# Performance work log

Hardware: AMD Instinct MI355X
Metric: run time of the kernel (lower is better)

## Reference

```python
import jax, jax.numpy as jnp
import numpy as np

N_NODES = 100000
N_EDGES = 600000
NUM_RELS = 6
NUM_BASES = 6
DIMS = [26, 64, 128, 32]  # in_features -> hidden[0] -> hidden[1] -> X_dim


def _layer(h, etypes, src, dst, V, C, S, b):
    """One basis-decomposed RGCN layer (DGL RelGraphConv semantics).
    h: [N, in]; V: [num_bases, in, out]; C: [num_rels, num_bases];
    S: self-loop weight [in, out]; b: bias [out].
    """
    # compose relation weights from bases: [num_rels, in, out]
    W = jnp.einsum('rb,bio->rio', C, V)
    # transform every node by every relation (cheaper than per-edge [E,in,out])
    h_rel = jnp.einsum('ni,rio->rno', h, W)          # [num_rels, N, out]
    msg = h_rel[etypes, src]                          # [E, out] gather
    agg = jax.ops.segment_sum(msg, dst, num_segments=h.shape[0])  # scatter-add
    return jax.nn.relu(agg + h @ S + b)


def setup_inputs() -> dict:
    key = jax.random.key(0)
    ks = jax.random.split(key, 16)
    inp = {
        'node_feats': jax.random.normal(ks[0], (N_NODES, DIMS[0]), dtype=jnp.float32),
        'src': jax.random.randint(ks[1], (N_EDGES,), 0, N_NODES, dtype=jnp.int32),
        'dst': jax.random.randint(ks[2], (N_EDGES,), 0, N_NODES, dtype=jnp.int32),
        'etypes': jax.random.randint(ks[3], (N_EDGES,), 0, NUM_RELS, dtype=jnp.int32),
    }
    ki = 4
    for l in range(3):
        din, dout = DIMS[l], DIMS[l + 1]
        sc = 1.0 / np.sqrt(din)
        inp[f'V{l+1}'] = jax.random.normal(ks[ki], (NUM_BASES, din, dout), dtype=jnp.float32) * sc
        inp[f'C{l+1}'] = jax.random.normal(ks[ki+1], (NUM_RELS, NUM_BASES), dtype=jnp.float32) * (1.0 / np.sqrt(NUM_BASES))
        inp[f'S{l+1}'] = jax.random.normal(ks[ki+2], (din, dout), dtype=jnp.float32) * sc
        inp[f'b{l+1}'] = jnp.zeros((dout,), dtype=jnp.float32)
        ki += 3
    return inp


def reference(node_feats, src, dst, etypes,
              V1, C1, S1, b1, V2, C2, S2, b2, V3, C3, S3, b3):
    h = _layer(node_feats, etypes, src, dst, V1, C1, S1, b1)
    h = _layer(h, etypes, src, dst, V2, C2, S2, b2)
    h = _layer(h, etypes, src, dst, V3, C3, S3, b3)
    return h
```

## Files before the change

### kernel.cpp

```cpp
#include <hip/hip_runtime.h>

#define NN 100000
#define NE 600000
#define NR 6
#define NB 6
#define NKEY (NN * NR)
#define NCHUNK ((NKEY + 1023) / 1024)

typedef __attribute__((ext_vector_type(8))) short bfrag;
typedef __attribute__((ext_vector_type(8))) unsigned short uvec8;
typedef __attribute__((ext_vector_type(8))) unsigned char ucvec8;
typedef __attribute__((ext_vector_type(4))) float accvec;

__device__ __forceinline__ float bf2f(unsigned short u) {
  union { unsigned int i; float f; } v;
  v.i = ((unsigned int)u) << 16;
  return v.f;
}
__device__ __forceinline__ unsigned short f2bf(float f) {
  union { float f; unsigned int i; } v;
  v.f = f;
  return (unsigned short)((v.i + 0x7FFFu + ((v.i >> 16) & 1u)) >> 16);
}
__device__ __forceinline__ float fp82f(unsigned char u) {
  return __builtin_amdgcn_cvt_f32_fp8((unsigned int)u, 0);
}
__device__ __forceinline__ unsigned char f2fp8(float f) {
  return (unsigned char)(__builtin_amdgcn_cvt_pk_fp8_f32(f, 0.f, 0, false) & 0xff);
}

template <int IN, int OUT, int KS, int NT>
__device__ __forceinline__ void compose_body(int idx, const float* __restrict__ V,
                                             const float* __restrict__ C,
                                             const float* __restrict__ S,
                                             unsigned short* __restrict__ Wf) {
  int lane = idx & 63;
  int t = idx >> 6;
  int nt = t % NT; t /= NT;
  int ks = t % KS; int rel = t / KS;
  int n = nt * 16 + (lane & 15);
  int g = lane >> 4;
  uvec8 o;
#pragma unroll
  for (int i = 0; i < 8; ++i) {
    int k = ks * 32 + g * 8 + i;
    float s = 0.f;
    if (k < IN) {
      if (rel < NR) {
#pragma unroll
        for (int b = 0; b < NB; ++b) s += C[rel * NB + b] * V[((size_t)b * IN + k) * OUT + n];
      } else {
        s = S[(size_t)k * OUT + n];
      }
    }
    o[i] = f2bf(s);
  }
  *(uvec8*)&Wf[(size_t)idx * 8] = o;
}

#define PB_PAD 1563
#define PB_HIST 2344
__global__ __launch_bounds__(256) void prep_kernel(
    const float* __restrict__ nf, unsigned short* __restrict__ hp,
    const int* __restrict__ dst, const int* __restrict__ et, int* __restrict__ cnt,
    const float* V1, const float* C1, const float* S1, unsigned short* W1,
    const float* V2, const float* C2, const float* S2, unsigned short* W2,
    const float* V3, const float* C3, const float* S3, unsigned short* W3) {
  int b = blockIdx.x, tid = threadIdx.x;
  if (b < PB_PAD) {
    int idx = b * 256 + tid;
    if (idx < NN * 4) {
      int n = idx >> 2, c = idx & 3;
      uvec8 o;
#pragma unroll
      for (int i = 0; i < 8; ++i) {
        int k = c * 8 + i;
        o[i] = (k < 26) ? f2bf(nf[n * 26 + k]) : (unsigned short)0;
      }
      *(uvec8*)&hp[(size_t)n * 32 + c * 8] = o;
    }
  } else if (b < PB_PAD + PB_HIST) {
    int e = (b - PB_PAD) * 256 + tid;
    if (e < NE) atomicAdd(&cnt[dst[e] * NR + et[e]], 1);
  } else if (b < PB_PAD + PB_HIST + 7) {
    int idx = (b - PB_PAD - PB_HIST) * 256 + tid;
    compose_body<26, 64, 1, 4>(idx, V1, C1, S1, W1);
  } else if (b < PB_PAD + PB_HIST + 7 + 28) {
    int idx = (b - PB_PAD - PB_HIST - 7) * 256 + tid;
    compose_body<64, 128, 2, 8>(idx, V2, C2, S2, W2);
  } else {
    int idx = (b - PB_PAD - PB_HIST - 35) * 256 + tid;
    compose_body<128, 32, 4, 2>(idx, V3, C3, S3, W3);
  }
}

__global__ void scanA(const int* __restrict__ cnt, int* __restrict__ partial) {
  __shared__ int ts[256];
  int t = threadIdx.x;
  int base = blockIdx.x * 1024 + t * 4;
  int s = 0;
#pragma unroll
  for (int i = 0; i < 4; ++i)
    if (base + i < NKEY) s += cnt[base + i];
  ts[t] = s;
  __syncthreads();
  for (int off = 128; off; off >>= 1) {
    if (t < off) ts[t] += ts[t + off];
    __syncthreads();
  }
  if (t == 0) partial[blockIdx.x] = ts[0];
}

__global__ void scanC2(int* __restrict__ cnt, const int* __restrict__ partial,
                       int* __restrict__ indptr) {
  __shared__ int ts[256];
  int t = threadIdx.x;
  int bid = blockIdx.x;
  int ps = 0;
  for (int i = t; i < bid; i += 256) ps += partial[i];
  ts[t] = ps;
  __syncthreads();
  for (int off = 128; off; off >>= 1) {
    if (t < off) ts[t] += ts[t + off];
    __syncthreads();
  }
  int base = ts[0];
  __syncthreads();

  int bbase = bid * 1024 + t * 4;
  int v[4], s = 0;
#pragma unroll
  for (int i = 0; i < 4; ++i) {
    v[i] = (bbase + i < NKEY) ? cnt[bbase + i] : 0;
    s += v[i];
  }
  ts[t] = s;
  __syncthreads();
  for (int off = 1; off < 256; off <<= 1) {
    int x = (t >= off) ? ts[t - off] : 0;
    __syncthreads();
    ts[t] += x;
    __syncthreads();
  }
  int run = base + ts[t] - s;
#pragma unroll
  for (int i = 0; i < 4; ++i) {
    if (bbase + i < NKEY) {
      indptr[bbase + i] = run;
      cnt[bbase + i] = run;
      run += v[i];
    }
  }
  if (bid == 0 && t == 0) indptr[NKEY] = NE;
}

__global__ void scatter2(const int* __restrict__ et, const int* __restrict__ src,
                         const int* __restrict__ dst, int* __restrict__ cur,
                         int* __restrict__ sidx, int* __restrict__ gidx) {
  int e = blockIdx.x * 256 + threadIdx.x;
  if (e < NE) {
    int r = et[e];
    int s = src[e];
    int key = dst[e] * NR + r;
    int pos = atomicAdd(&cur[key], 1);
    sidx[pos] = s;
    gidx[pos] = r * NN + s;
  }
}

template <int K, int OUT, int MAXE, bool IN_FP8, bool OUT_FP8>
__global__ __launch_bounds__(256, 8) void rgcn_layer_v6(
    const void* __restrict__ hv,
    const unsigned short* __restrict__ Wf,
    const float* __restrict__ bias,
    const int* __restrict__ indptr,
    const int* __restrict__ sidx,
    void* __restrict__ Gout) {
  constexpr int ROWS = 16;
  constexpr int KS = K / 32;
  constexpr int KT = 7 * KS;
  constexpr int NT = OUT / 16;
  constexpr int NTW = NT / 4;
  constexpr int KC = K / 8;
  constexpr int CT = 7 * KC;
  constexpr int ITEMS = (ROWS * CT + 255) / 256;
  constexpr int KP = 7 * K + 8;
  constexpr int MSB = IN_FP8 ? (K + 8) : (2 * K + 16);
  constexpr int ATB = ROWS * KP * 2;
  constexpr int MGB = MAXE * MSB;
  constexpr int LDSB = ATB > MGB ? ATB : MGB;
  constexpr int SITER = MAXE * KC / 256;

  __shared__ __align__(16) char buf[LDSB];
  __shared__ int seg[ROWS * NR + 1];
  unsigned short* A = (unsigned short*)buf;

  const int tid = threadIdx.x;
  const int row0 = blockIdx.x * ROWS;

  if (tid < ROWS * NR + 1) seg[tid] = indptr[row0 * NR + tid];
  __syncthreads();

  const int E0 = seg[0];
  const int E1 = seg[ROWS * NR];

  float sum[ITEMS][8];
#pragma unroll
  for (int i = 0; i < ITEMS; ++i)
#pragma unroll
    for (int q = 0; q < 8; ++q) sum[i][q] = 0.f;

  for (int b0 = E0; b0 < E1; b0 += MAXE) {
    const int bcount = min(MAXE, E1 - b0);
    __syncthreads();

#pragma unroll
    for (int i = 0; i < SITER; ++i) {
      int idx = tid + i * 256;
      int e = idx / KC;
      int c = idx & (KC - 1);
      int ec = min(e, bcount - 1);
      int s = sidx[b0 + ec];
      if constexpr (IN_FP8) {
        *(ucvec8*)&buf[e * MSB + c * 8] =
            *(const ucvec8*)((const unsigned char*)hv + (size_t)s * K + c * 8);
      } else {
        *(uvec8*)&buf[e * MSB + c * 16] =
            *(const uvec8*)((const unsigned short*)hv + (size_t)s * K + c * 8);
      }
    }
    __syncthreads();

#pragma unroll
    for (int i = 0; i < ITEMS; ++i) {
      int idx = tid + i * 256;
      if (idx < ROWS * CT) {
        int row = idx / CT, chunk = idx % CT;
        if (chunk < 6 * KC) {
          int rel = chunk / KC, c = chunk & (KC - 1);
          int beg = seg[row * NR + rel], end = seg[row * NR + rel + 1];
          int lo = max(beg, b0), hi = min(end, b0 + bcount);
          for (int e = lo; e < hi; ++e) {
            if constexpr (IN_FP8) {
              ucvec8 t = *(const ucvec8*)&buf[(e - b0) * MSB + c * 8];
#pragma unroll
              for (int q = 0; q < 8; ++q) sum[i][q] += fp82f(t[q]);
            } else {
              uvec8 t = *(const uvec8*)&buf[(e - b0) * MSB + c * 16];
#pragma unroll
              for (int q = 0; q < 8; ++q) sum[i][q] += bf2f(t[q]);
            }
          }
        }
      }
    }
  }

  __syncthreads();

#pragma unroll
  for (int i = 0; i < ITEMS; ++i) {
    int idx = tid + i * 256;
    if (idx < ROWS * CT) {
      int row = idx / CT, chunk = idx % CT;
      uvec8 o;
      if (chunk >= 6 * KC) {
        int c = chunk - 6 * KC;
        if constexpr (IN_FP8) {
          ucvec8 tv = *(const ucvec8*)((const unsigned char*)hv +
                                       (size_t)(row0 + row) * K + c * 8);
#pragma unroll
          for (int q = 0; q < 8; ++q) o[q] = f2bf(fp82f(tv[q]));
        } else {
          o = *(const uvec8*)((const unsigned short*)hv + (size_t)(row0 + row) * K + c * 8);
        }
      } else {
#pragma unroll
        for (int q = 0; q < 8; ++q) o[q] = f2bf(sum[i][q]);
      }
      *(uvec8*)&A[row * KP + chunk * 8] = o;
    }
  }
  __syncthreads();

  const int lane = tid & 63;
  const int wv = tid >> 6;
  const int abase = (lane & 15) * KP + (lane >> 4) * 8;

  accvec acc[NTW];
#pragma unroll
  for (int j = 0; j < NTW; ++j) acc[j] = 0.f;

#pragma unroll
  for (int kst = 0; kst < KT; ++kst) {
    bfrag af = *(const bfrag*)&A[abase + kst * 32];
#pragma unroll
    for (int j = 0; j < NTW; ++j) {
      int nt = wv * NTW + j;
      bfrag bf = *(const bfrag*)&Wf[(size_t)((kst * NT + nt) * 64 + lane) * 8];
      acc[j] = __builtin_amdgcn_mfma_f32_16x16x32_bf16(af, bf, acc[j], 0, 0, 0);
    }
  }

  const int r0 = row0 + (lane >> 4) * 4;
  const int col0 = lane & 15;
#pragma unroll
  for (int j = 0; j < NTW; ++j) {
    int c = (wv * NTW + j) * 16 + col0;
    float bv = bias[c];
#pragma unroll
    for (int r = 0; r < 4; ++r) {
      float v = fmaxf(acc[j][r] + bv, 0.f);
      if constexpr (OUT_FP8)
        ((unsigned char*)Gout)[(size_t)(r0 + r) * OUT + c] = f2fp8(v);
      else
        ((unsigned short*)Gout)[(size_t)(r0 + r) * OUT + c] = f2bf(v);
    }
  }
}

template <int K, int OUT>
__global__ __launch_bounds__(256, 4) void rgcn_transform(
    const unsigned short* __restrict__ h,
    const unsigned short* __restrict__ Wf,
    unsigned short* __restrict__ Y) {
  constexpr int KS = K / 32;
  constexpr int NT = OUT / 16;
  constexpr int KC = K / 8;
  constexpr int KP = K + 8;

  __shared__ unsigned short Asm[64 * KP];
  const int tid = threadIdx.x;
  const int row0 = blockIdx.x * 64;

  for (int idx = tid; idx < 64 * KC; idx += 256) {
    int j = idx / KC, c = idx - (idx / KC) * KC;
    int row = row0 + j;
    uvec8 o = 0;
    if (row < NN) o = *(const uvec8*)&h[(size_t)row * K + c * 8];
    *(uvec8*)&Asm[j * KP + c * 8] = o;
  }
  __syncthreads();

  const int lane = tid & 63;
  const int wv = tid >> 6;
  const int abase = (wv * 16 + (lane & 15)) * KP + (lane >> 4) * 8;

  bfrag af[KS];
#pragma unroll
  for (int ks = 0; ks < KS; ++ks) af[ks] = *(const bfrag*)&Asm[abase + ks * 32];

  const int r0 = row0 + wv * 16 + (lane >> 4) * 4;
  const int col0 = lane & 15;

  for (int rel = 0; rel <= NR; ++rel) {
    accvec acc[NT];
#pragma unroll
    for (int nt = 0; nt < NT; ++nt) acc[nt] = 0.f;
    const unsigned short* Wr = Wf + (size_t)rel * KS * NT * 512;
#pragma unroll
    for (int ks = 0; ks < KS; ++ks) {
#pragma unroll
      for (int nt = 0; nt < NT; ++nt) {
        bfrag bf = *(const bfrag*)&Wr[(size_t)((ks * NT + nt) * 64 + lane) * 8];
        acc[nt] = __builtin_amdgcn_mfma_f32_16x16x32_bf16(af[ks], bf, acc[nt], 0, 0, 0);
      }
    }
#pragma unroll
    for (int nt = 0; nt < NT; ++nt) {
      int c = nt * 16 + col0;
#pragma unroll
      for (int r = 0; r < 4; ++r) {
        int row = r0 + r;
        if (row < NN)
          Y[((size_t)rel * NN + row) * OUT + c] = f2bf(acc[nt][r]);
      }
    }
  }
}

__global__ __launch_bounds__(256, 8) void rgcn_agg3(
    const unsigned short* __restrict__ Y,
    const int* __restrict__ indptr,
    const int* __restrict__ gidx,
    const float* __restrict__ bias,
    float* __restrict__ out) {
  int t = blockIdx.x * 256 + threadIdx.x;
  int row = t >> 2;
  if (row >= NN) return;
  int c = (t & 3) * 8;

  int beg = indptr[row * NR];
  int end = indptr[row * NR + NR];

  float s[8] = {0.f, 0.f, 0.f, 0.f, 0.f, 0.f, 0.f, 0.f};
  int e = beg;
  for (; e + 3 < end; e += 4) {
    int g0 = gidx[e], g1 = gidx[e + 1], g2 = gidx[e + 2], g3 = gidx[e + 3];
    uvec8 v0 = *(const uvec8*)&Y[(size_t)g0 * 32 + c];
    uvec8 v1 = *(const uvec8*)&Y[(size_t)g1 * 32 + c];
    uvec8 v2 = *(const uvec8*)&Y[(size_t)g2 * 32 + c];
    uvec8 v3 = *(const uvec8*)&Y[(size_t)g3 * 32 + c];
#pragma unroll
    for (int i = 0; i < 8; ++i)
      s[i] += (bf2f(v0[i]) + bf2f(v1[i])) + (bf2f(v2[i]) + bf2f(v3[i]));
  }
  for (; e < end; ++e) {
    int g = gidx[e];
    uvec8 v = *(const uvec8*)&Y[(size_t)g * 32 + c];
#pragma unroll
    for (int i = 0; i < 8; ++i) s[i] += bf2f(v[i]);
  }
  uvec8 vs = *(const uvec8*)&Y[((size_t)NR * NN + row) * 32 + c];
#pragma unroll
  for (int i = 0; i < 8; ++i) s[i] += bf2f(vs[i]);

  float4 o0, o1;
  o0.x = fmaxf(s[0] + bias[c + 0], 0.f);
  o0.y = fmaxf(s[1] + bias[c + 1], 0.f);
  o0.z = fmaxf(s[2] + bias[c + 2], 0.f);
  o0.w = fmaxf(s[3] + bias[c + 3], 0.f);
  o1.x = fmaxf(s[4] + bias[c + 4], 0.f);
  o1.y = fmaxf(s[5] + bias[c + 5], 0.f);
  o1.z = fmaxf(s[6] + bias[c + 6], 0.f);
  o1.w = fmaxf(s[7] + bias[c + 7], 0.f);
  *(float4*)&out[(size_t)row * 32 + c] = o0;
  *(float4*)&out[(size_t)row * 32 + c + 4] = o1;
}

static inline char* align_up(char* p, size_t a) {
  return (char*)(((size_t)p + a - 1) & ~(a - 1));
}

extern "C" void kernel_launch(void* const* d_in, const int* in_sizes, int n_in,
                              void* d_out, int out_size, void* d_ws, size_t ws_size,
                              hipStream_t stream) {
  const float* nf = (const float*)d_in[0];
  const int* src  = (const int*)d_in[1];
  const int* dst  = (const int*)d_in[2];
  const int* et   = (const int*)d_in[3];
  const float* V1 = (const float*)d_in[4];
  const float* C1 = (const float*)d_in[5];
  const float* S1 = (const float*)d_in[6];
  const float* b1 = (const float*)d_in[7];
  const float* V2 = (const float*)d_in[8];
  const float* C2 = (const float*)d_in[9];
  const float* S2 = (const float*)d_in[10];
  const float* b2 = (const float*)d_in[11];
  const float* V3 = (const float*)d_in[12];
  const float* C3 = (const float*)d_in[13];
  const float* S3 = (const float*)d_in[14];
  const float* b3 = (const float*)d_in[15];
  float* out = (float*)d_out;

  constexpr int WF1 = (NR + 1) * 1 * 4 * 512;
  constexpr int WF2 = (NR + 1) * 2 * 8 * 512;
  constexpr int WF3 = (NR + 1) * 4 * 2 * 512;

  char* p = (char*)d_ws;
  int* cnt = (int*)p;                p = align_up(p + (size_t)NKEY * 4, 256);
  int* indptr = (int*)p;             p = align_up(p + (size_t)(NKEY + 1) * 4, 256);
  int* partial = (int*)p;            p = align_up(p + (size_t)NCHUNK * 4, 256);
  int* sidx = (int*)p;               p = align_up(p + (size_t)NE * 4, 256);
  int* gidx = (int*)p;               p = align_up(p + (size_t)NE * 4, 256);
  unsigned short* hp = (unsigned short*)p;  p = align_up(p + (size_t)NN * 32 * 2, 256);
  unsigned short* W1 = (unsigned short*)p;  p = align_up(p + (size_t)WF1 * 2, 256);
  unsigned short* W2 = (unsigned short*)p;  p = align_up(p + (size_t)WF2 * 2, 256);
  unsigned short* W3 = (unsigned short*)p;  p = align_up(p + (size_t)WF3 * 2, 256);
  unsigned char* G1 = (unsigned char*)p;    p = align_up(p + (size_t)NN * 64, 256);
  unsigned short* G2 = (unsigned short*)p;  p = align_up(p + (size_t)NN * 128 * 2, 256);
  unsigned short* Y3 = (unsigned short*)p;  p = align_up(p + (size_t)(NR + 1) * NN * 32 * 2, 256);

  hipMemsetAsync(cnt, 0, (size_t)NKEY * 4, stream);

  const int EB = (NE + 255) / 256;
  prep_kernel<<<PB_PAD + PB_HIST + 49, 256, 0, stream>>>(
      nf, hp, dst, et, cnt, V1, C1, S1, W1, V2, C2, S2, W2, V3, C3, S3, W3);
  scanA<<<NCHUNK, 256, 0, stream>>>(cnt, partial);
  scanC2<<<NCHUNK, 256, 0, stream>>>(cnt, partial, indptr);
  scatter2<<<EB, 256, 0, stream>>>(et, src, dst, cnt, sidx, gidx);

  const int NB16 = NN / 16;
  rgcn_layer_v6<32, 64, 128, false, true><<<NB16, 256, 0, stream>>>(
      hp, W1, b1, indptr, sidx, G1);
  rgcn_layer_v6<64, 128, 128, true, false><<<NB16, 256, 0, stream>>>(
      G1, W2, b2, indptr, sidx, G2);

  const int NBK = (NN + 63) / 64;
  rgcn_transform<128, 32><<<NBK, 256, 0, stream>>>(G2, W3, Y3);
  rgcn_agg3<<<(NN * 4 + 255) / 256, 256, 0, stream>>>(Y3, indptr, gidx, b3, out);

  (void)in_sizes; (void)n_in; (void)out_size; (void)ws_size;
}
```

Before: 184.1 us.

## Aggregate edges with LDS float atomics using packed edge records

The scatter step now packs source node, relation and local destination row into one edge record. Each layer kernel then walks the block's edges flat, gathers the source features and atomically adds them into an fp32 LDS tile. This replaces the staged batch copy and the per-(row, relation) serial reduction, which suffered from load imbalance. The intermediate G1 goes back to bf16 instead of fp8, and the conversion uses a packed bf16 convert instruction. In exchange the code takes on LDS atomic contention, a larger fp32 tile that lowers occupancy in layer 2, and twice the bytes for G1.

```diff
diff --git a/kernel.cpp b/kernel.cpp
--- a/kernel.cpp
+++ b/kernel.cpp
@@ -9,7 +9,6 @@
 
 typedef __attribute__((ext_vector_type(8))) short bfrag;
 typedef __attribute__((ext_vector_type(8))) unsigned short uvec8;
-typedef __attribute__((ext_vector_type(8))) unsigned char ucvec8;
 typedef __attribute__((ext_vector_type(4))) float accvec;
 
 __device__ __forceinline__ float bf2f(unsigned short u) {
@@ -22,11 +21,10 @@
   v.f = f;
   return (unsigned short)((v.i + 0x7FFFu + ((v.i >> 16) & 1u)) >> 16);
 }
-__device__ __forceinline__ float fp82f(unsigned char u) {
-  return __builtin_amdgcn_cvt_f32_fp8((unsigned int)u, 0);
-}
-__device__ __forceinline__ unsigned char f2fp8(float f) {
-  return (unsigned char)(__builtin_amdgcn_cvt_pk_fp8_f32(f, 0.f, 0, false) & 0xff);
+__device__ __forceinline__ unsigned int cvtpk_bf16(float lo, float hi) {
+  unsigned int r;
+  asm("v_cvt_pk_bf16_f32 %0, %1, %2" : "=v"(r) : "v"(lo), "v"(hi));
+  return r;
 }
 
 template <int IN, int OUT, int KS, int NT>
@@ -156,129 +154,112 @@
 
 __global__ void scatter2(const int* __restrict__ et, const int* __restrict__ src,
                          const int* __restrict__ dst, int* __restrict__ cur,
-                         int* __restrict__ sidx, int* __restrict__ gidx) {
+                         int* __restrict__ erec, int* __restrict__ gidx) {
   int e = blockIdx.x * 256 + threadIdx.x;
   if (e < NE) {
     int r = et[e];
     int s = src[e];
-    int key = dst[e] * NR + r;
+    int d = dst[e];
+    int key = d * NR + r;
     int pos = atomicAdd(&cur[key], 1);
-    sidx[pos] = s;
+    erec[pos] = s | (r << 17) | ((d & 15) << 20);
     gidx[pos] = r * NN + s;
   }
 }
 
-template <int K, int OUT, int MAXE, bool IN_FP8, bool OUT_FP8>
-__global__ __launch_bounds__(256, 8) void rgcn_layer_v6(
-    const void* __restrict__ hv,
+template <int K, int OUT, int WPE>
+__global__ __launch_bounds__(256, WPE) void rgcn_layer_v7(
+    const unsigned short* __restrict__ h,
     const unsigned short* __restrict__ Wf,
     const float* __restrict__ bias,
     const int* __restrict__ indptr,
-    const int* __restrict__ sidx,
-    void* __restrict__ Gout) {
+    const int* __restrict__ erec,
+    unsigned short* __restrict__ Gout) {
   constexpr int ROWS = 16;
   constexpr int KS = K / 32;
   constexpr int KT = 7 * KS;
   constexpr int NT = OUT / 16;
   constexpr int NTW = NT / 4;
   constexpr int KC = K / 8;
+  constexpr int LKC = (KC == 4) ? 2 : 3;
   constexpr int CT = 7 * KC;
   constexpr int ITEMS = (ROWS * CT + 255) / 256;
+  constexpr int KPF = 7 * K + 4;
   constexpr int KP = 7 * K + 8;
-  constexpr int MSB = IN_FP8 ? (K + 8) : (2 * K + 16);
-  constexpr int ATB = ROWS * KP * 2;
-  constexpr int MGB = MAXE * MSB;
-  constexpr int LDSB = ATB > MGB ? ATB : MGB;
-  constexpr int SITER = MAXE * KC / 256;
-
-  __shared__ __align__(16) char buf[LDSB];
-  __shared__ int seg[ROWS * NR + 1];
-  unsigned short* A = (unsigned short*)buf;
+
+  __shared__ __align__(16) float A32[ROWS * KPF];
+  unsigned short* A16 = (unsigned short*)A32;
 
   const int tid = threadIdx.x;
   const int row0 = blockIdx.x * ROWS;
 
-  if (tid < ROWS * NR + 1) seg[tid] = indptr[row0 * NR + tid];
-  __syncthreads();
-
-  const int E0 = seg[0];
-  const int E1 = seg[ROWS * NR];
-
-  float sum[ITEMS][8];
-#pragma unroll
-  for (int i = 0; i < ITEMS; ++i)
-#pragma unroll
-    for (int q = 0; q < 8; ++q) sum[i][q] = 0.f;
-
-  for (int b0 = E0; b0 < E1; b0 += MAXE) {
-    const int bcount = min(MAXE, E1 - b0);
-    __syncthreads();
-
-#pragma unroll
-    for (int i = 0; i < SITER; ++i) {
-      int idx = tid + i * 256;
-      int e = idx / KC;
-      int c = idx & (KC - 1);
-      int ec = min(e, bcount - 1);
-      int s = sidx[b0 + ec];
-      if constexpr (IN_FP8) {
-        *(ucvec8*)&buf[e * MSB + c * 8] =
-            *(const ucvec8*)((const unsigned char*)hv + (size_t)s * K + c * 8);
-      } else {
-        *(uvec8*)&buf[e * MSB + c * 16] =
-            *(const uvec8*)((const unsigned short*)hv + (size_t)s * K + c * 8);
-      }
-    }
-    __syncthreads();
-
-#pragma unroll
-    for (int i = 0; i < ITEMS; ++i) {
-      int idx = tid + i * 256;
-      if (idx < ROWS * CT) {
-        int row = idx / CT, chunk = idx % CT;
-        if (chunk < 6 * KC) {
-          int rel = chunk / KC, c = chunk & (KC - 1);
-          int beg = seg[row * NR + rel], end = seg[row * NR + rel + 1];
-          int lo = max(beg, b0), hi = min(end, b0 + bcount);
-          for (int e = lo; e < hi; ++e) {
-            if constexpr (IN_FP8) {
-              ucvec8 t = *(const ucvec8*)&buf[(e - b0) * MSB + c * 8];
-#pragma unroll
-              for (int q = 0; q < 8; ++q) sum[i][q] += fp82f(t[q]);
-            } else {
-              uvec8 t = *(const uvec8*)&buf[(e - b0) * MSB + c * 16];
-#pragma unroll
-              for (int q = 0; q < 8; ++q) sum[i][q] += bf2f(t[q]);
-            }
-          }
-        }
-      }
-    }
-  }
-
-  __syncthreads();
+  const int E0 = indptr[row0 * NR];
+  const int E1 = indptr[(row0 + ROWS) * NR];
 
 #pragma unroll
   for (int i = 0; i < ITEMS; ++i) {
     int idx = tid + i * 256;
     if (idx < ROWS * CT) {
       int row = idx / CT, chunk = idx % CT;
-      uvec8 o;
+      float4 a = make_float4(0.f, 0.f, 0.f, 0.f), b = a;
       if (chunk >= 6 * KC) {
         int c = chunk - 6 * KC;
-        if constexpr (IN_FP8) {
-          ucvec8 tv = *(const ucvec8*)((const unsigned char*)hv +
-                                       (size_t)(row0 + row) * K + c * 8);
-#pragma unroll
-          for (int q = 0; q < 8; ++q) o[q] = f2bf(fp82f(tv[q]));
-        } else {
-          o = *(const uvec8*)((const unsigned short*)hv + (size_t)(row0 + row) * K + c * 8);
-        }
-      } else {
-#pragma unroll
-        for (int q = 0; q < 8; ++q) o[q] = f2bf(sum[i][q]);
+        uvec8 t = *(const uvec8*)&h[(size_t)(row0 + row) * K + c * 8];
+        a.x = bf2f(t[0]); a.y = bf2f(t[1]); a.z = bf2f(t[2]); a.w = bf2f(t[3]);
+        b.x = bf2f(t[4]); b.y = bf2f(t[5]); b.z = bf2f(t[6]); b.w = bf2f(t[7]);
       }
-      *(uvec8*)&A[row * KP + chunk * 8] = o;
+      float* d = &A32[row * KPF + chunk * 8];
+      *(float4*)d = a;
+      *(float4*)(d + 4) = b;
+    }
+  }
+  __syncthreads();
+
+  {
+    const int nit = (E1 - E0) * KC;
+    auto body = [&](int idx) {
+      int e = idx >> LKC;
+      int c = idx & (KC - 1);
+      unsigned rec = (unsigned)erec[E0 + e];
+      int s = rec & 0x1FFFF;
+      int rel = (rec >> 17) & 7;
+      int row = (int)(rec >> 20);
+      uvec8 t = *(const uvec8*)&h[(size_t)s * K + c * 8];
+      float* d = &A32[row * KPF + rel * K + c * 8];
+#pragma unroll
+      for (int q = 0; q < 8; ++q) atomicAdd(&d[q], bf2f(t[q]));
+    };
+    int idx = tid;
+    for (; idx + 256 < nit; idx += 512) { body(idx); body(idx + 256); }
+    if (idx < nit) body(idx);
+  }
+  __syncthreads();
+
+  float rv[ITEMS][8];
+#pragma unroll
+  for (int i = 0; i < ITEMS; ++i) {
+    int idx = tid + i * 256;
+    if (idx < ROWS * CT) {
+      int row = idx / CT, chunk = idx % CT;
+      const float* s = &A32[row * KPF + chunk * 8];
+      float4 a = *(const float4*)s;
+      float4 b = *(const float4*)(s + 4);
+      rv[i][0] = a.x; rv[i][1] = a.y; rv[i][2] = a.z; rv[i][3] = a.w;
+      rv[i][4] = b.x; rv[i][5] = b.y; rv[i][6] = b.z; rv[i][7] = b.w;
+    }
+  }
+  __syncthreads();
+#pragma unroll
+  for (int i = 0; i < ITEMS; ++i) {
+    int idx = tid + i * 256;
+    if (idx < ROWS * CT) {
+      int row = idx / CT, chunk = idx % CT;
+      uint4 w;
+      w.x = cvtpk_bf16(rv[i][0], rv[i][1]);
+      w.y = cvtpk_bf16(rv[i][2], rv[i][3]);
+      w.z = cvtpk_bf16(rv[i][4], rv[i][5]);
+      w.w = cvtpk_bf16(rv[i][6], rv[i][7]);
+      *(uint4*)&A16[row * KP + chunk * 8] = w;
     }
   }
   __syncthreads();
@@ -293,7 +274,7 @@
 
 #pragma unroll
   for (int kst = 0; kst < KT; ++kst) {
-    bfrag af = *(const bfrag*)&A[abase + kst * 32];
+    bfrag af = *(const bfrag*)&A16[abase + kst * 32];
 #pragma unroll
     for (int j = 0; j < NTW; ++j) {
       int nt = wv * NTW + j;
@@ -311,10 +292,7 @@
 #pragma unroll
     for (int r = 0; r < 4; ++r) {
       float v = fmaxf(acc[j][r] + bv, 0.f);
-      if constexpr (OUT_FP8)
-        ((unsigned char*)Gout)[(size_t)(r0 + r) * OUT + c] = f2fp8(v);
-      else
-        ((unsigned short*)Gout)[(size_t)(r0 + r) * OUT + c] = f2bf(v);
+      Gout[(size_t)(r0 + r) * OUT + c] = f2bf(v);
     }
   }
 }
@@ -461,13 +439,13 @@
   int* cnt = (int*)p;                p = align_up(p + (size_t)NKEY * 4, 256);
   int* indptr = (int*)p;             p = align_up(p + (size_t)(NKEY + 1) * 4, 256);
   int* partial = (int*)p;            p = align_up(p + (size_t)NCHUNK * 4, 256);
-  int* sidx = (int*)p;               p = align_up(p + (size_t)NE * 4, 256);
+  int* erec = (int*)p;               p = align_up(p + (size_t)NE * 4, 256);
   int* gidx = (int*)p;               p = align_up(p + (size_t)NE * 4, 256);
   unsigned short* hp = (unsigned short*)p;  p = align_up(p + (size_t)NN * 32 * 2, 256);
   unsigned short* W1 = (unsigned short*)p;  p = align_up(p + (size_t)WF1 * 2, 256);
   unsigned short* W2 = (unsigned short*)p;  p = align_up(p + (size_t)WF2 * 2, 256);
   unsigned short* W3 = (unsigned short*)p;  p = align_up(p + (size_t)WF3 * 2, 256);
-  unsigned char* G1 = (unsigned char*)p;    p = align_up(p + (size_t)NN * 64, 256);
+  unsigned short* G1 = (unsigned short*)p;  p = align_up(p + (size_t)NN * 64 * 2, 256);
   unsigned short* G2 = (unsigned short*)p;  p = align_up(p + (size_t)NN * 128 * 2, 256);
   unsigned short* Y3 = (unsigned short*)p;  p = align_up(p + (size_t)(NR + 1) * NN * 32 * 2, 256);
 
@@ -478,13 +456,11 @@
       nf, hp, dst, et, cnt, V1, C1, S1, W1, V2, C2, S2, W2, V3, C3, S3, W3);
   scanA<<<NCHUNK, 256, 0, stream>>>(cnt, partial);
   scanC2<<<NCHUNK, 256, 0, stream>>>(cnt, partial, indptr);
-  scatter2<<<EB, 256, 0, stream>>>(et, src, dst, cnt, sidx, gidx);
+  scatter2<<<EB, 256, 0, stream>>>(et, src, dst, cnt, erec, gidx);
 
   const int NB16 = NN / 16;
-  rgcn_layer_v6<32, 64, 128, false, true><<<NB16, 256, 0, stream>>>(
-      hp, W1, b1, indptr, sidx, G1);
-  rgcn_layer_v6<64, 128, 128, true, false><<<NB16, 256, 0, stream>>>(
-      G1, W2, b2, indptr, sidx, G2);
+  rgcn_layer_v7<32, 64, 8><<<NB16, 256, 0, stream>>>(hp, W1, b1, indptr, erec, G1);
+  rgcn_layer_v7<64, 128, 5><<<NB16, 256, 0, stream>>>(G1, W2, b2, indptr, erec, G2);
 
   const int NBK = (NN + 63) / 64;
   rgcn_transform<128, 32><<<NBK, 256, 0, stream>>>(G2, W3, Y3);
```

After: 456.5 us. 148% more time.

## Fuse layer-3 transform into layer-2 kernel, pack edge records, drop fp8 intermediates

Applied to the files above, without the earlier changes.

Layer 2's output tile is kept in shared memory and immediately multiplied by the seven layer-3 weight blocks inside the same kernel. This removes the separate transform kernel and the global write and read of the 100000x128 G2 buffer. The src and etype indices are packed into a single int per edge, replacing the separate sidx and gidx arrays and cutting index traffic. G1 is now bf16 instead of fp8, which doubles its gather bytes but drops the fp8 conversions, and fp32 to bf16 packing uses v_cvt_pk_bf16_f32.

```diff
diff --git a/kernel.cpp b/kernel.cpp
--- a/kernel.cpp
+++ b/kernel.cpp
@@ -9,7 +9,6 @@
 
 typedef __attribute__((ext_vector_type(8))) short bfrag;
 typedef __attribute__((ext_vector_type(8))) unsigned short uvec8;
-typedef __attribute__((ext_vector_type(8))) unsigned char ucvec8;
 typedef __attribute__((ext_vector_type(4))) float accvec;
 
 __device__ __forceinline__ float bf2f(unsigned short u) {
@@ -22,11 +21,10 @@
   v.f = f;
   return (unsigned short)((v.i + 0x7FFFu + ((v.i >> 16) & 1u)) >> 16);
 }
-__device__ __forceinline__ float fp82f(unsigned char u) {
-  return __builtin_amdgcn_cvt_f32_fp8((unsigned int)u, 0);
-}
-__device__ __forceinline__ unsigned char f2fp8(float f) {
-  return (unsigned char)(__builtin_amdgcn_cvt_pk_fp8_f32(f, 0.f, 0, false) & 0xff);
+__device__ __forceinline__ unsigned int cvtpk_bf16(float lo, float hi) {
+  unsigned int r;
+  asm("v_cvt_pk_bf16_f32 %0, %1, %2" : "=v"(r) : "v"(lo), "v"(hi));
+  return r;
 }
 
 template <int IN, int OUT, int KS, int NT>
@@ -156,44 +154,45 @@
 
 __global__ void scatter2(const int* __restrict__ et, const int* __restrict__ src,
                          const int* __restrict__ dst, int* __restrict__ cur,
-                         int* __restrict__ sidx, int* __restrict__ gidx) {
+                         int* __restrict__ erec) {
   int e = blockIdx.x * 256 + threadIdx.x;
   if (e < NE) {
     int r = et[e];
     int s = src[e];
     int key = dst[e] * NR + r;
     int pos = atomicAdd(&cur[key], 1);
-    sidx[pos] = s;
-    gidx[pos] = r * NN + s;
-  }
-}
-
-template <int K, int OUT, int MAXE, bool IN_FP8, bool OUT_FP8>
-__global__ __launch_bounds__(256, 8) void rgcn_layer_v6(
-    const void* __restrict__ hv,
+    erec[pos] = s | (r << 17);
+  }
+}
+
+template <int K, int OUT, int MAXE, bool FUSE3>
+__global__ __launch_bounds__(256, 8) void rgcn_layer_v8(
+    const unsigned short* __restrict__ h,
     const unsigned short* __restrict__ Wf,
     const float* __restrict__ bias,
     const int* __restrict__ indptr,
-    const int* __restrict__ sidx,
-    void* __restrict__ Gout) {
+    const int* __restrict__ erec,
+    unsigned short* __restrict__ Gout,
+    const unsigned short* __restrict__ Wf3,
+    unsigned short* __restrict__ Y3) {
   constexpr int ROWS = 16;
   constexpr int KS = K / 32;
   constexpr int KT = 7 * KS;
   constexpr int NT = OUT / 16;
   constexpr int NTW = NT / 4;
   constexpr int KC = K / 8;
+  constexpr int LKC = (KC == 4) ? 2 : 3;
   constexpr int CT = 7 * KC;
   constexpr int ITEMS = (ROWS * CT + 255) / 256;
   constexpr int KP = 7 * K + 8;
-  constexpr int MSB = IN_FP8 ? (K + 8) : (2 * K + 16);
-  constexpr int ATB = ROWS * KP * 2;
-  constexpr int MGB = MAXE * MSB;
-  constexpr int LDSB = ATB > MGB ? ATB : MGB;
+  constexpr int MSU = K + 8;
+  constexpr int ATE = ROWS * KP;
+  constexpr int MGE = MAXE * MSU;
+  constexpr int LDSE = ATE > MGE ? ATE : MGE;
   constexpr int SITER = MAXE * KC / 256;
 
-  __shared__ __align__(16) char buf[LDSB];
+  __shared__ __align__(16) unsigned short A16[LDSE];
   __shared__ int seg[ROWS * NR + 1];
-  unsigned short* A = (unsigned short*)buf;
 
   const int tid = threadIdx.x;
   const int row0 = blockIdx.x * ROWS;
@@ -217,17 +216,11 @@
 #pragma unroll
     for (int i = 0; i < SITER; ++i) {
       int idx = tid + i * 256;
-      int e = idx / KC;
+      int e = idx >> LKC;
       int c = idx & (KC - 1);
       int ec = min(e, bcount - 1);
-      int s = sidx[b0 + ec];
-      if constexpr (IN_FP8) {
-        *(ucvec8*)&buf[e * MSB + c * 8] =
-            *(const ucvec8*)((const unsigned char*)hv + (size_t)s * K + c * 8);
-      } else {
-        *(uvec8*)&buf[e * MSB + c * 16] =
-            *(const uvec8*)((const unsigned short*)hv + (size_t)s * K + c * 8);
-      }
+      int s = erec[b0 + ec] & 0x1FFFF;
+      *(uvec8*)&A16[e * MSU + c * 8] = *(const uvec8*)&h[(size_t)s * K + c * 8];
     }
     __syncthreads();
 
@@ -237,19 +230,13 @@
       if (idx < ROWS * CT) {
         int row = idx / CT, chunk = idx % CT;
         if (chunk < 6 * KC) {
-          int rel = chunk / KC, c = chunk & (KC - 1);
+          int rel = chunk >> LKC, c = chunk & (KC - 1);
           int beg = seg[row * NR + rel], end = seg[row * NR + rel + 1];
           int lo = max(beg, b0), hi = min(end, b0 + bcount);
           for (int e = lo; e < hi; ++e) {
-            if constexpr (IN_FP8) {
-              ucvec8 t = *(const ucvec8*)&buf[(e - b0) * MSB + c * 8];
-#pragma unroll
-              for (int q = 0; q < 8; ++q) sum[i][q] += fp82f(t[q]);
-            } else {
-              uvec8 t = *(const uvec8*)&buf[(e - b0) * MSB + c * 16];
-#pragma unroll
-              for (int q = 0; q < 8; ++q) sum[i][q] += bf2f(t[q]);
-            }
+            uvec8 t = *(const uvec8*)&A16[(e - b0) * MSU + c * 8];
+#pragma unroll
+            for (int q = 0; q < 8; ++q) sum[i][q] += bf2f(t[q]);
           }
         }
       }
@@ -263,22 +250,17 @@
     int idx = tid + i * 256;
     if (idx < ROWS * CT) {
       int row = idx / CT, chunk = idx % CT;
-      uvec8 o;
+      uint4 w;
       if (chunk >= 6 * KC) {
         int c = chunk - 6 * KC;
-        if constexpr (IN_FP8) {
-          ucvec8 tv = *(const ucvec8*)((const unsigned char*)hv +
-                                       (size_t)(row0 + row) * K + c * 8);
-#pragma unroll
-          for (int q = 0; q < 8; ++q) o[q] = f2bf(fp82f(tv[q]));
-        } else {
-          o = *(const uvec8*)((const unsigned short*)hv + (size_t)(row0 + row) * K + c * 8);
-        }
+        w = *(const uint4*)&h[(size_t)(row0 + row) * K + c * 8];
       } else {
-#pragma unroll
-        for (int q = 0; q < 8; ++q) o[q] = f2bf(sum[i][q]);
-      }
-      *(uvec8*)&A[row * KP + chunk * 8] = o;
+        w.x = cvtpk_bf16(sum[i][0], sum[i][1]);
+        w.y = cvtpk_bf16(sum[i][2], sum[i][3]);
+        w.z = cvtpk_bf16(sum[i][4], sum[i][5]);
+        w.w = cvtpk_bf16(sum[i][6], sum[i][7]);
+      }
+      *(uint4*)&A16[row * KP + chunk * 8] = w;
     }
   }
   __syncthreads();
@@ -293,7 +275,7 @@
 
 #pragma unroll
   for (int kst = 0; kst < KT; ++kst) {
-    bfrag af = *(const bfrag*)&A[abase + kst * 32];
+    bfrag af = *(const bfrag*)&A16[abase + kst * 32];
 #pragma unroll
     for (int j = 0; j < NTW; ++j) {
       int nt = wv * NTW + j;
@@ -302,78 +284,59 @@
     }
   }
 
-  const int r0 = row0 + (lane >> 4) * 4;
+  const int lr0 = (lane >> 4) * 4;
   const int col0 = lane & 15;
-#pragma unroll
-  for (int j = 0; j < NTW; ++j) {
-    int c = (wv * NTW + j) * 16 + col0;
-    float bv = bias[c];
-#pragma unroll
-    for (int r = 0; r < 4; ++r) {
-      float v = fmaxf(acc[j][r] + bv, 0.f);
-      if constexpr (OUT_FP8)
-        ((unsigned char*)Gout)[(size_t)(r0 + r) * OUT + c] = f2fp8(v);
-      else
-        ((unsigned short*)Gout)[(size_t)(r0 + r) * OUT + c] = f2bf(v);
-    }
-  }
-}
-
-template <int K, int OUT>
-__global__ __launch_bounds__(256, 4) void rgcn_transform(
-    const unsigned short* __restrict__ h,
-    const unsigned short* __restrict__ Wf,
-    unsigned short* __restrict__ Y) {
-  constexpr int KS = K / 32;
-  constexpr int NT = OUT / 16;
-  constexpr int KC = K / 8;
-  constexpr int KP = K + 8;
-
-  __shared__ unsigned short Asm[64 * KP];
-  const int tid = threadIdx.x;
-  const int row0 = blockIdx.x * 64;
-
-  for (int idx = tid; idx < 64 * KC; idx += 256) {
-    int j = idx / KC, c = idx - (idx / KC) * KC;
-    int row = row0 + j;
-    uvec8 o = 0;
-    if (row < NN) o = *(const uvec8*)&h[(size_t)row * K + c * 8];
-    *(uvec8*)&Asm[j * KP + c * 8] = o;
-  }
-  __syncthreads();
-
-  const int lane = tid & 63;
-  const int wv = tid >> 6;
-  const int abase = (wv * 16 + (lane & 15)) * KP + (lane >> 4) * 8;
-
-  bfrag af[KS];
-#pragma unroll
-  for (int ks = 0; ks < KS; ++ks) af[ks] = *(const bfrag*)&Asm[abase + ks * 32];
-
-  const int r0 = row0 + wv * 16 + (lane >> 4) * 4;
-  const int col0 = lane & 15;
-
-  for (int rel = 0; rel <= NR; ++rel) {
-    accvec acc[NT];
-#pragma unroll
-    for (int nt = 0; nt < NT; ++nt) acc[nt] = 0.f;
-    const unsigned short* Wr = Wf + (size_t)rel * KS * NT * 512;
-#pragma unroll
-    for (int ks = 0; ks < KS; ++ks) {
-#pragma unroll
-      for (int nt = 0; nt < NT; ++nt) {
-        bfrag bf = *(const bfrag*)&Wr[(size_t)((ks * NT + nt) * 64 + lane) * 8];
-        acc[nt] = __builtin_amdgcn_mfma_f32_16x16x32_bf16(af[ks], bf, acc[nt], 0, 0, 0);
-      }
-    }
-#pragma unroll
-    for (int nt = 0; nt < NT; ++nt) {
-      int c = nt * 16 + col0;
+
+  if constexpr (!FUSE3) {
+#pragma unroll
+    for (int j = 0; j < NTW; ++j) {
+      int c = (wv * NTW + j) * 16 + col0;
+      float bv = bias[c];
 #pragma unroll
       for (int r = 0; r < 4; ++r) {
-        int row = r0 + r;
-        if (row < NN)
-          Y[((size_t)rel * NN + row) * OUT + c] = f2bf(acc[nt][r]);
+        float v = fmaxf(acc[j][r] + bv, 0.f);
+        Gout[(size_t)(row0 + lr0 + r) * OUT + c] = f2bf(v);
+      }
+    }
+  } else {
+    constexpr int GP = 136;
+    __syncthreads();
+#pragma unroll
+    for (int j = 0; j < NTW; ++j) {
+      int c = (wv * NTW + j) * 16 + col0;
+      float bv = bias[c];
+#pragma unroll
+      for (int r = 0; r < 4; ++r)
+        A16[(lr0 + r) * GP + c] = f2bf(fmaxf(acc[j][r] + bv, 0.f));
+    }
+    __syncthreads();
+
+    const int abase2 = (lane & 15) * GP + (lane >> 4) * 8;
+    bfrag a2[4];
+#pragma unroll
+    for (int ks = 0; ks < 4; ++ks) a2[ks] = *(const bfrag*)&A16[abase2 + ks * 32];
+
+#pragma unroll
+    for (int rr = 0; rr < 2; ++rr) {
+      int rel = wv + rr * 4;
+      if (rel < 7) {
+        accvec y[2];
+        y[0] = 0.f; y[1] = 0.f;
+#pragma unroll
+        for (int ks = 0; ks < 4; ++ks) {
+#pragma unroll
+          for (int nt = 0; nt < 2; ++nt) {
+            bfrag bf = *(const bfrag*)&Wf3[(size_t)(((rel * 4 + ks) * 2 + nt) * 64 + lane) * 8];
+            y[nt] = __builtin_amdgcn_mfma_f32_16x16x32_bf16(a2[ks], bf, y[nt], 0, 0, 0);
+          }
+        }
+#pragma unroll
+        for (int nt = 0; nt < 2; ++nt) {
+          int c = nt * 16 + col0;
+#pragma unroll
+          for (int r = 0; r < 4; ++r)
+            Y3[((size_t)rel * NN + row0 + lr0 + r) * 32 + c] = f2bf(y[nt][r]);
+        }
       }
     }
   }
@@ -382,7 +345,7 @@
 __global__ __launch_bounds__(256, 8) void rgcn_agg3(
     const unsigned short* __restrict__ Y,
     const int* __restrict__ indptr,
-    const int* __restrict__ gidx,
+    const int* __restrict__ erec,
     const float* __restrict__ bias,
     float* __restrict__ out) {
   int t = blockIdx.x * 256 + threadIdx.x;
@@ -396,18 +359,23 @@
   float s[8] = {0.f, 0.f, 0.f, 0.f, 0.f, 0.f, 0.f, 0.f};
   int e = beg;
   for (; e + 3 < end; e += 4) {
-    int g0 = gidx[e], g1 = gidx[e + 1], g2 = gidx[e + 2], g3 = gidx[e + 3];
-    uvec8 v0 = *(const uvec8*)&Y[(size_t)g0 * 32 + c];
-    uvec8 v1 = *(const uvec8*)&Y[(size_t)g1 * 32 + c];
-    uvec8 v2 = *(const uvec8*)&Y[(size_t)g2 * 32 + c];
-    uvec8 v3 = *(const uvec8*)&Y[(size_t)g3 * 32 + c];
+    unsigned r0 = erec[e], r1 = erec[e + 1], r2 = erec[e + 2], r3 = erec[e + 3];
+    size_t g0 = (size_t)(r0 >> 17) * NN + (r0 & 0x1FFFF);
+    size_t g1 = (size_t)(r1 >> 17) * NN + (r1 & 0x1FFFF);
+    size_t g2 = (size_t)(r2 >> 17) * NN + (r2 & 0x1FFFF);
+    size_t g3 = (size_t)(r3 >> 17) * NN + (r3 & 0x1FFFF);
+    uvec8 v0 = *(const uvec8*)&Y[g0 * 32 + c];
+    uvec8 v1 = *(const uvec8*)&Y[g1 * 32 + c];
+    uvec8 v2 = *(const uvec8*)&Y[g2 * 32 + c];
+    uvec8 v3 = *(const uvec8*)&Y[g3 * 32 + c];
 #pragma unroll
     for (int i = 0; i < 8; ++i)
       s[i] += (bf2f(v0[i]) + bf2f(v1[i])) + (bf2f(v2[i]) + bf2f(v3[i]));
   }
   for (; e < end; ++e) {
-    int g = gidx[e];
-    uvec8 v = *(const uvec8*)&Y[(size_t)g * 32 + c];
+    unsigned r = erec[e];
+    size_t g = (size_t)(r >> 17) * NN + (r & 0x1FFFF);
+    uvec8 v = *(const uvec8*)&Y[g * 32 + c];
 #pragma unroll
     for (int i = 0; i < 8; ++i) s[i] += bf2f(v[i]);
   }
@@ -461,14 +429,12 @@
   int* cnt = (int*)p;                p = align_up(p + (size_t)NKEY * 4, 256);
   int* indptr = (int*)p;             p = align_up(p + (size_t)(NKEY + 1) * 4, 256);
   int* partial = (int*)p;            p = align_up(p + (size_t)NCHUNK * 4, 256);
-  int* sidx = (int*)p;               p = align_up(p + (size_t)NE * 4, 256);
-  int* gidx = (int*)p;               p = align_up(p + (size_t)NE * 4, 256);
+  int* erec = (int*)p;               p = align_up(p + (size_t)NE * 4, 256);
   unsigned short* hp = (unsigned short*)p;  p = align_up(p + (size_t)NN * 32 * 2, 256);
   unsigned short* W1 = (unsigned short*)p;  p = align_up(p + (size_t)WF1 * 2, 256);
   unsigned short* W2 = (unsigned short*)p;  p = align_up(p + (size_t)WF2 * 2, 256);
   unsigned short* W3 = (unsigned short*)p;  p = align_up(p + (size_t)WF3 * 2, 256);
-  unsigned char* G1 = (unsigned char*)p;    p = align_up(p + (size_t)NN * 64, 256);
-  unsigned short* G2 = (unsigned short*)p;  p = align_up(p + (size_t)NN * 128 * 2, 256);
+  unsigned short* G1 = (unsigned short*)p;  p = align_up(p + (size_t)NN * 64 * 2, 256);
   unsigned short* Y3 = (unsigned short*)p;  p = align_up(p + (size_t)(NR + 1) * NN * 32 * 2, 256);
 
   hipMemsetAsync(cnt, 0, (size_t)NKEY * 4, stream);
@@ -478,17 +444,15 @@
       nf, hp, dst, et, cnt, V1, C1, S1, W1, V2, C2, S2, W2, V3, C3, S3, W3);
   scanA<<<NCHUNK, 256, 0, stream>>>(cnt, partial);
   scanC2<<<NCHUNK, 256, 0, stream>>>(cnt, partial, indptr);
-  scatter2<<<EB, 256, 0, stream>>>(et, src, dst, cnt, sidx, gidx);
+  scatter2<<<EB, 256, 0, stream>>>(et, src, dst, cnt, erec);
 
   const int NB16 = NN / 16;
-  rgcn_layer_v6<32, 64, 128, false, true><<<NB16, 256, 0, stream>>>(
-      hp, W1, b1, indptr, sidx, G1);
-  rgcn_layer_v6<64, 128, 128, true, false><<<NB16, 256, 0, stream>>>(
-      G1, W2, b2, indptr, sidx, G2);
-
-  const int NBK = (NN + 63) / 64;
-  rgcn_transform<128, 32><<<NBK, 256, 0, stream>>>(G2, W3, Y3);
-  rgcn_agg3<<<(NN * 4 + 255) / 256, 256, 0, stream>>>(Y3, indptr, gidx, b3, out);
+  rgcn_layer_v8<32, 64, 128, false><<<NB16, 256, 0, stream>>>(
+      hp, W1, b1, indptr, erec, G1, nullptr, nullptr);
+  rgcn_layer_v8<64, 128, 128, true><<<NB16, 256, 0, stream>>>(
+      G1, W2, b2, indptr, erec, nullptr, W3, Y3);
+
+  rgcn_agg3<<<(NN * 4 + 255) / 256, 256, 0, stream>>>(Y3, indptr, erec, b3, out);
 
   (void)in_sizes; (void)n_in; (void)out_size; (void)ws_size;
 }
```

Result: faster. 172.0 us (-6.6%).
